# Optimization experiments

Measured on AMD Instinct MI355X. Metric: run time of the kernel, lower is better.

The kernel has to match this reference:

```python
import jax, jax.numpy as jnp
import numpy as np

KSIZE = 5
DILATION = 1
DYN = 32  # dynamic (value) channels


def setup_inputs() -> dict:
    key = jax.random.key(0)
    k1, k2 = jax.random.split(key)
    x = jax.random.normal(k1, (4, 64, 256, 256), dtype=jnp.float32)
    kernel = jax.random.normal(k2, (KSIZE * KSIZE, 1), dtype=jnp.float32)
    return {"input": x, "kernel": kernel}


def _neighborhoods(x):
    """Gather KxK dilated neighborhoods with zero padding.
    x: [B, C, H, W] -> [B, C, K^2, H, W], taps in row-major (i, j) order
    matching nn.Unfold."""
    B, C, H, W = x.shape
    pad = DILATION * (KSIZE // 2)
    xp = jnp.pad(x, ((0, 0), (0, 0), (pad, pad), (pad, pad)))
    taps = [xp[:, :, i * DILATION:i * DILATION + H, j * DILATION:j * DILATION + W]
            for i in range(KSIZE) for j in range(KSIZE)]
    return jnp.stack(taps, axis=2)


def reference(input, kernel):
    x = input
    nbrs = _neighborhoods(x)                      # [B, C, K2, H, W]
    # scores over static channels (c >= DYN) against center pixel, scaled by
    # learned per-tap kernel weight / kernel_size
    scores = jnp.einsum('bckhw,bchw->bkhw', nbrs[:, DYN:], x[:, DYN:])
    scores = scores * (kernel[:, 0][None, :, None, None] / KSIZE)
    smax = jax.nn.softmax(scores, axis=1)          # softmax over K^2 taps
    # weighted sum of dynamic channels
    out = jnp.einsum('bkhw,bckhw->bchw', smax, nbrs[:, :DYN])
    return out
```

## Files before the change

kernel.cpp:

```cpp
#include <hip/hip_runtime.h>
#include <math.h>

#define KS    5
#define K2    25
#define BB    4
#define HH    256
#define WW    256
#define PLANE (HH * WW)
#define LROWD 264
#define PTILE 1864
#define NTHR  256

typedef __attribute__((ext_vector_type(2))) _Float16 half2_t;

static __device__ __forceinline__ half2_t u2h(unsigned u) { return __builtin_bit_cast(half2_t, u); }

static __device__ __forceinline__ unsigned pkrtz(float a, float b) {
    auto h = __builtin_amdgcn_cvt_pkrtz(a, b);
    return __builtin_bit_cast(unsigned, h);
}

static __device__ __forceinline__ float dot2(half2_t a, half2_t b, float c) {
#if __has_builtin(__builtin_amdgcn_fdot2)
    return __builtin_amdgcn_fdot2(a, b, c, false);
#else
    return (float)a.x * (float)b.x + ((float)a.y * (float)b.y + c);
#endif
}

__global__ __launch_bounds__(NTHR, 2)
void local_attn_kernel(const float* __restrict__ x,
                       const float* __restrict__ kern,
                       float* __restrict__ out)
{
    __shared__ unsigned ldsu[2 * 4 * PTILE];
    __shared__ float kw[K2];

    const int tid = threadIdx.x;
    for (int i = tid; i < 2 * 4 * PTILE; i += NTHR) ldsu[i] = 0u;
    if (tid < K2) kw[tid] = kern[tid] * (1.0f / KS);

    const int lane = tid & 63;
    const int wv   = tid >> 6;
    const int ty   = wv >> 1;
    const int cg   = lane >> 5;
    const int tx   = ((wv & 1) << 5) | (lane & 31);
    const int w0   = tx << 2;

    const int bx     = blockIdx.x;
    const int hgroup = ((bx & 7) << 4) | (bx >> 3);
    const int h0     = hgroup * 2;
    const int h      = h0 + ty;
    const int b      = blockIdx.y;

    const float* xb = x + (size_t)b * 64 * PLANE;

    int gofs[6], lofs[6], pofs[6];
#pragma unroll
    for (int i = 0; i < 6; ++i) {
        const int rp   = (tid >> 6) + 4 * i;
        const int row  = rp % 6;
        const int pair = rp / 6;
        const int r    = h0 - 2 + row;
        const bool v   = (unsigned)r < (unsigned)HH;
        gofs[i] = min(max(r, 0), HH - 1) * WW + (tid & 63) * 4;
        pofs[i] = pair * 2 * PLANE;
        lofs[i] = pair * PTILE + (v ? row : 6) * LROWD + 2 + (tid & 63) * 4;
    }

    float4 pa[6], pb[6];
    auto prefetch = [&](int st) {
        const float* xc = xb + (size_t)((st < 4) ? 32 + st * 8 : (st - 4) * 8) * PLANE;
#pragma unroll
        for (int i = 0; i < 6; ++i) {
            pa[i] = *(const float4*)(xc + pofs[i] + gofs[i]);
            pb[i] = *(const float4*)(xc + pofs[i] + PLANE + gofs[i]);
        }
    };
    auto cvtwrite = [&](int bufi) {
        unsigned* lb = ldsu + bufi * 4 * PTILE;
#pragma unroll
        for (int i = 0; i < 6; ++i) {
            const unsigned d0 = pkrtz(pa[i].x, pb[i].x);
            const unsigned d1 = pkrtz(pa[i].y, pb[i].y);
            const unsigned d2 = pkrtz(pa[i].z, pb[i].z);
            const unsigned d3 = pkrtz(pa[i].w, pb[i].w);
            *(uint2*)(lb + lofs[i])     = make_uint2(d0, d1);
            *(uint2*)(lb + lofs[i] + 2) = make_uint2(d2, d3);
        }
    };

    float s[4][K2];
#pragma unroll
    for (int p = 0; p < 4; ++p)
#pragma unroll
        for (int k = 0; k < K2; ++k) s[p][k] = 0.0f;

    __syncthreads();
    prefetch(0);
    cvtwrite(0);
    __syncthreads();

#pragma unroll 1
    for (int t = 0; t < 8; ++t) {
        if (t + 1 < 8) prefetch(t + 1);
        const unsigned* buf = ldsu + (t & 1) * 4 * PTILE;

        if (t < 4) {
#pragma unroll
            for (int dp = 0; dp < 2; ++dp) {
                const unsigned* tb = buf + (cg * 2 + dp) * PTILE;
                half2_t ctr[4];
                {
                    const unsigned* rp = tb + (ty + 2) * LROWD + w0;
                    const uint4 r0 = *(const uint4*)(rp);
                    const uint4 r1 = *(const uint4*)(rp + 4);
                    half2_t f[8] = {u2h(r0.x), u2h(r0.y), u2h(r0.z), u2h(r0.w),
                                    u2h(r1.x), u2h(r1.y), u2h(r1.z), u2h(r1.w)};
#pragma unroll
                    for (int p = 0; p < 4; ++p) ctr[p] = f[p + 2];
#pragma unroll
                    for (int j = 0; j < KS; ++j)
#pragma unroll
                        for (int p = 0; p < 4; ++p)
                            s[p][2 * KS + j] = dot2(f[p + j], ctr[p], s[p][2 * KS + j]);
                }
#pragma unroll
                for (int i = 0; i < KS; ++i) {
                    if (i == 2) continue;
                    const unsigned* rp = tb + (ty + i) * LROWD + w0;
                    const uint4 r0 = *(const uint4*)(rp);
                    const uint4 r1 = *(const uint4*)(rp + 4);
                    half2_t f[8] = {u2h(r0.x), u2h(r0.y), u2h(r0.z), u2h(r0.w),
                                    u2h(r1.x), u2h(r1.y), u2h(r1.z), u2h(r1.w)};
#pragma unroll
                    for (int j = 0; j < KS; ++j)
#pragma unroll
                        for (int p = 0; p < 4; ++p)
                            s[p][i * KS + j] = dot2(f[p + j], ctr[p], s[p][i * KS + j]);
                }
            }
            if (t == 3) {
#pragma unroll
                for (int p = 0; p < 4; ++p)
#pragma unroll
                    for (int k = 0; k < K2; ++k)
                        s[p][k] += __shfl_xor(s[p][k], 32, 64);
#pragma unroll
                for (int p = 0; p < 4; ++p) {
                    float mx = -INFINITY;
#pragma unroll
                    for (int k = 0; k < K2; ++k) {
                        float v = s[p][k] * kw[k];
                        s[p][k] = v;
                        mx = fmaxf(mx, v);
                    }
                    float sum = 0.0f;
#pragma unroll
                    for (int k = 0; k < K2; ++k) {
                        float e = __expf(s[p][k] - mx);
                        s[p][k] = e;
                        sum += e;
                    }
                    const float inv = 1.0f / sum;
#pragma unroll
                    for (int k = 0; k < K2; ++k) s[p][k] *= inv;
                }
            }
        } else {
            const int chb = (t - 4) * 8;
#pragma unroll
            for (int dp = 0; dp < 2; ++dp) {
                const unsigned* tb = buf + (cg * 2 + dp) * PTILE;
                float alo[4] = {0.f, 0.f, 0.f, 0.f};
                float ahi[4] = {0.f, 0.f, 0.f, 0.f};
#pragma unroll
                for (int i = 0; i < KS; ++i) {
                    const unsigned* rp = tb + (ty + i) * LROWD + w0;
                    const uint4 r0 = *(const uint4*)(rp);
                    const uint4 r1 = *(const uint4*)(rp + 4);
                    half2_t f[8] = {u2h(r0.x), u2h(r0.y), u2h(r0.z), u2h(r0.w),
                                    u2h(r1.x), u2h(r1.y), u2h(r1.z), u2h(r1.w)};
#pragma unroll
                    for (int j = 0; j < KS; ++j)
#pragma unroll
                        for (int p = 0; p < 4; ++p) {
                            const half2_t v = f[p + j];
                            const float  wgt = s[p][i * KS + j];
                            alo[p] = fmaf((float)v.x, wgt, alo[p]);
                            ahi[p] = fmaf((float)v.y, wgt, ahi[p]);
                        }
                }
                const int c0 = chb + (cg * 2 + dp) * 2;
                float* op = out + ((size_t)b * 32 + c0) * PLANE + h * WW + w0;
                *(float4*)op           = make_float4(alo[0], alo[1], alo[2], alo[3]);
                *(float4*)(op + PLANE) = make_float4(ahi[0], ahi[1], ahi[2], ahi[3]);
            }
        }

        if (t + 1 < 8) {
            cvtwrite((t + 1) & 1);
            __syncthreads();
        }
    }
}

extern "C" void kernel_launch(void* const* d_in, const int* in_sizes, int n_in,
                              void* d_out, int out_size, void* d_ws, size_t ws_size,
                              hipStream_t stream) {
    const float* x    = (const float*)d_in[0];
    const float* kern = (const float*)d_in[1];
    float*       out  = (float*)d_out;

    dim3 grid(HH / 2, BB, 1);
    dim3 block(NTHR, 1, 1);
    hipLaunchKernelGGL(local_attn_kernel, grid, block, 0, stream, x, kern, out);
}
```

Measured before the change: 113.7 us.

## Double threads per block and halve pixels per thread to raise occupancy

Moves from 256 to 512 threads per block, with each thread handling 2 horizontal pixels instead of 4. The per-thread score array, global prefetch registers and LDS read widths shrink to match, and launch bounds now ask for 4 blocks per CU. The aim is more waves in flight to hide LDS and global latency. In exchange, neighbouring threads re-read more overlapping halo data from LDS and issue narrower float2 stores.

Result: slower. 137.1 us (+20.6%).

```diff
diff --git a/kernel.cpp b/kernel.cpp
--- a/kernel.cpp
+++ b/kernel.cpp
@@ -9,7 +9,7 @@
 #define PLANE (HH * WW)
 #define LROWD 264
 #define PTILE 1864
-#define NTHR  256
+#define NTHR  512
 
 typedef __attribute__((ext_vector_type(2))) _Float16 half2_t;
 
@@ -28,7 +28,7 @@
 #endif
 }
 
-__global__ __launch_bounds__(NTHR, 2)
+__global__ __launch_bounds__(NTHR, 4)
 void local_attn_kernel(const float* __restrict__ x,
                        const float* __restrict__ kern,
                        float* __restrict__ out)
@@ -42,10 +42,10 @@
 
     const int lane = tid & 63;
     const int wv   = tid >> 6;
-    const int ty   = wv >> 1;
+    const int ty   = wv >> 2;
     const int cg   = lane >> 5;
-    const int tx   = ((wv & 1) << 5) | (lane & 31);
-    const int w0   = tx << 2;
+    const int tx   = ((wv & 3) << 5) | (lane & 31);
+    const int w0   = tx << 1;
 
     const int bx     = blockIdx.x;
     const int hgroup = ((bx & 7) << 4) | (bx >> 3);
@@ -55,10 +55,10 @@
 
     const float* xb = x + (size_t)b * 64 * PLANE;
 
-    int gofs[6], lofs[6], pofs[6];
-#pragma unroll
-    for (int i = 0; i < 6; ++i) {
-        const int rp   = (tid >> 6) + 4 * i;
+    int gofs[3], lofs[3], pofs[3];
+#pragma unroll
+    for (int i = 0; i < 3; ++i) {
+        const int rp   = (tid >> 6) + 8 * i;
         const int row  = rp % 6;
         const int pair = rp / 6;
         const int r    = h0 - 2 + row;
@@ -68,11 +68,11 @@
         lofs[i] = pair * PTILE + (v ? row : 6) * LROWD + 2 + (tid & 63) * 4;
     }
 
-    float4 pa[6], pb[6];
+    float4 pa[3], pb[3];
     auto prefetch = [&](int st) {
         const float* xc = xb + (size_t)((st < 4) ? 32 + st * 8 : (st - 4) * 8) * PLANE;
 #pragma unroll
-        for (int i = 0; i < 6; ++i) {
+        for (int i = 0; i < 3; ++i) {
             pa[i] = *(const float4*)(xc + pofs[i] + gofs[i]);
             pb[i] = *(const float4*)(xc + pofs[i] + PLANE + gofs[i]);
         }
@@ -80,7 +80,7 @@
     auto cvtwrite = [&](int bufi) {
         unsigned* lb = ldsu + bufi * 4 * PTILE;
 #pragma unroll
-        for (int i = 0; i < 6; ++i) {
+        for (int i = 0; i < 3; ++i) {
             const unsigned d0 = pkrtz(pa[i].x, pb[i].x);
             const unsigned d1 = pkrtz(pa[i].y, pb[i].y);
             const unsigned d2 = pkrtz(pa[i].z, pb[i].z);
@@ -90,9 +90,9 @@
         }
     };
 
-    float s[4][K2];
-#pragma unroll
-    for (int p = 0; p < 4; ++p)
+    float s[2][K2];
+#pragma unroll
+    for (int p = 0; p < 2; ++p)
 #pragma unroll
         for (int k = 0; k < K2; ++k) s[p][k] = 0.0f;
 
@@ -110,44 +110,46 @@
 #pragma unroll
             for (int dp = 0; dp < 2; ++dp) {
                 const unsigned* tb = buf + (cg * 2 + dp) * PTILE;
-                half2_t ctr[4];
+                half2_t ctr[2];
                 {
                     const unsigned* rp = tb + (ty + 2) * LROWD + w0;
-                    const uint4 r0 = *(const uint4*)(rp);
-                    const uint4 r1 = *(const uint4*)(rp + 4);
-                    half2_t f[8] = {u2h(r0.x), u2h(r0.y), u2h(r0.z), u2h(r0.w),
-                                    u2h(r1.x), u2h(r1.y), u2h(r1.z), u2h(r1.w)};
-#pragma unroll
-                    for (int p = 0; p < 4; ++p) ctr[p] = f[p + 2];
+                    const uint2 r0 = *(const uint2*)(rp);
+                    const uint2 r1 = *(const uint2*)(rp + 2);
+                    const uint2 r2 = *(const uint2*)(rp + 4);
+                    half2_t f[6] = {u2h(r0.x), u2h(r0.y), u2h(r1.x),
+                                    u2h(r1.y), u2h(r2.x), u2h(r2.y)};
+                    ctr[0] = f[2];
+                    ctr[1] = f[3];
 #pragma unroll
                     for (int j = 0; j < KS; ++j)
 #pragma unroll
-                        for (int p = 0; p < 4; ++p)
+                        for (int p = 0; p < 2; ++p)
                             s[p][2 * KS + j] = dot2(f[p + j], ctr[p], s[p][2 * KS + j]);
                 }
 #pragma unroll
                 for (int i = 0; i < KS; ++i) {
                     if (i == 2) continue;
                     const unsigned* rp = tb + (ty + i) * LROWD + w0;
-                    const uint4 r0 = *(const uint4*)(rp);
-                    const uint4 r1 = *(const uint4*)(rp + 4);
-                    half2_t f[8] = {u2h(r0.x), u2h(r0.y), u2h(r0.z), u2h(r0.w),
-                                    u2h(r1.x), u2h(r1.y), u2h(r1.z), u2h(r1.w)};
+                    const uint2 r0 = *(const uint2*)(rp);
+                    const uint2 r1 = *(const uint2*)(rp + 2);
+                    const uint2 r2 = *(const uint2*)(rp + 4);
+                    half2_t f[6] = {u2h(r0.x), u2h(r0.y), u2h(r1.x),
+                                    u2h(r1.y), u2h(r2.x), u2h(r2.y)};
 #pragma unroll
                     for (int j = 0; j < KS; ++j)
 #pragma unroll
-                        for (int p = 0; p < 4; ++p)
+                        for (int p = 0; p < 2; ++p)
                             s[p][i * KS + j] = dot2(f[p + j], ctr[p], s[p][i * KS + j]);
                 }
             }
             if (t == 3) {
 #pragma unroll
-                for (int p = 0; p < 4; ++p)
+                for (int p = 0; p < 2; ++p)
 #pragma unroll
                     for (int k = 0; k < K2; ++k)
                         s[p][k] += __shfl_xor(s[p][k], 32, 64);
 #pragma unroll
-                for (int p = 0; p < 4; ++p) {
+                for (int p = 0; p < 2; ++p) {
                     float mx = -INFINITY;
 #pragma unroll
                     for (int k = 0; k < K2; ++k) {
@@ -172,19 +174,20 @@
 #pragma unroll
             for (int dp = 0; dp < 2; ++dp) {
                 const unsigned* tb = buf + (cg * 2 + dp) * PTILE;
-                float alo[4] = {0.f, 0.f, 0.f, 0.f};
-                float ahi[4] = {0.f, 0.f, 0.f, 0.f};
+                float alo[2] = {0.f, 0.f};
+                float ahi[2] = {0.f, 0.f};
 #pragma unroll
                 for (int i = 0; i < KS; ++i) {
                     const unsigned* rp = tb + (ty + i) * LROWD + w0;
-                    const uint4 r0 = *(const uint4*)(rp);
-                    const uint4 r1 = *(const uint4*)(rp + 4);
-                    half2_t f[8] = {u2h(r0.x), u2h(r0.y), u2h(r0.z), u2h(r0.w),
-                                    u2h(r1.x), u2h(r1.y), u2h(r1.z), u2h(r1.w)};
+                    const uint2 r0 = *(const uint2*)(rp);
+                    const uint2 r1 = *(const uint2*)(rp + 2);
+                    const uint2 r2 = *(const uint2*)(rp + 4);
+                    half2_t f[6] = {u2h(r0.x), u2h(r0.y), u2h(r1.x),
+                                    u2h(r1.y), u2h(r2.x), u2h(r2.y)};
 #pragma unroll
                     for (int j = 0; j < KS; ++j)
 #pragma unroll
-                        for (int p = 0; p < 4; ++p) {
+                        for (int p = 0; p < 2; ++p) {
                             const half2_t v = f[p + j];
                             const float  wgt = s[p][i * KS + j];
                             alo[p] = fmaf((float)v.x, wgt, alo[p]);
@@ -193,8 +196,8 @@
                 }
                 const int c0 = chb + (cg * 2 + dp) * 2;
                 float* op = out + ((size_t)b * 32 + c0) * PLANE + h * WW + w0;
-                *(float4*)op           = make_float4(alo[0], alo[1], alo[2], alo[3]);
-                *(float4*)(op + PLANE) = make_float4(ahi[0], ahi[1], ahi[2], ahi[3]);
+                *(float2*)op           = make_float2(alo[0], alo[1]);
+                *(float2*)(op + PLANE) = make_float2(ahi[0], ahi[1]);
             }
         }
 
```
